# Performance work log

Hardware: AMD Instinct MI355X
Metric: run time of the kernel (lower is better)

## Reference

```python
import jax, jax.numpy as jnp
import numpy as np

# Module config (mirrors PlateYoloBlock __init__)
IMAGE_W, IMAGE_H = 2048, 2048
GRID_SIZE = 8
GRID_W = IMAGE_W // GRID_SIZE  # 256
GRID_H = IMAGE_H // GRID_SIZE  # 256
BBOX_ATTRS = 13


def _xy_offset():
    # np.meshgrid(arange(grid_w), arange(grid_h)) stacked on axis=2 -> (grid_h, grid_w, 2)
    # [..., 0] = x (column) index, [..., 1] = y (row) index
    gx = jnp.arange(GRID_W, dtype=jnp.float32)
    gy = jnp.arange(GRID_H, dtype=jnp.float32)
    xx, yy = jnp.meshgrid(gx, gy)  # each (grid_h, grid_w)
    return jnp.stack([xx, yy], axis=-1)  # (grid_h, grid_w, 2)


def setup_inputs() -> dict:
    key = jax.random.key(0)
    coordinates = jax.random.normal(key, (32, BBOX_ATTRS, GRID_H, GRID_W), dtype=jnp.float32)
    return {"coordinates": coordinates}


def reference(coordinates) -> jnp.ndarray:
    # Inference path of PlateYoloBlock.forward (target=None):
    #   permute (B,13,H,W) -> (B,H,W,13)
    #   xy   = sigmoid(raw[..., :2]) + grid offset
    #   wh   = exp(raw[..., 2:4])
    #   conf = sigmoid(raw[..., -1])
    #   all-but-conf scaled by grid_size; reshape to (B, grid_w*grid_h, 13)
    b = coordinates.shape[0]
    c = jnp.transpose(coordinates, (0, 2, 3, 1))  # (B, grid_h, grid_w, 13)
    xy = jax.nn.sigmoid(c[..., :2]) + _xy_offset()[None]  # (B,H,W,2)
    wh = jnp.exp(c[..., 2:4])
    corners = c[..., 4:12]  # raw 4-corner coords, untouched by activations
    conf = jax.nn.sigmoid(c[..., 12:13])
    boxes = jnp.concatenate([xy, wh, corners], axis=-1) * jnp.float32(GRID_SIZE)
    out = jnp.concatenate([boxes, conf], axis=-1)  # (B,H,W,13)
    return out.reshape(b, GRID_W * GRID_H, BBOX_ATTRS)
```

## Files before the change

kernel.cpp:

```cpp
#include <hip/hip_runtime.h>


#define NB      32
#define NC      13
#define HW      65536
#define WIDTH   256
#define TILE    512
#define THREADS 256

__device__ __forceinline__ float sigmoidf_(float x) {
    return 1.0f / (1.0f + __expf(-x));
}

__global__ __launch_bounds__(THREADS) void plate_yolo_kernel(
        const float* __restrict__ in, float* __restrict__ out) {
    __shared__ float lds[TILE * NC];

    const int tid = threadIdx.x;
    const long long s0 = (long long)blockIdx.x * TILE;
    const int b = (int)(s0 >> 16);
    const int posBase = (int)(s0 & (HW - 1));
    const float* __restrict__ inB = in + (long long)b * NC * HW + posBase;

    #pragma unroll
    for (int k = 0; k < TILE / THREADS; ++k) {
        const int p = tid + k * THREADS;
        const int pos = posBase + p;
        const float fx = (float)(pos & (WIDTH - 1));
        const float fy = (float)(pos >> 8);
        #pragma unroll
        for (int c = 0; c < NC; ++c) {
            float v = inB[c * HW + p];
            float r;
            if (c == 0)                 r = (sigmoidf_(v) + fx) * 8.0f;
            else if (c == 1)            r = (sigmoidf_(v) + fy) * 8.0f;
            else if (c == 2 || c == 3)  r = __expf(v) * 8.0f;
            else if (c == 12)           r = sigmoidf_(v);
            else                        r = v * 8.0f;
            lds[p * NC + c] = r;
        }
    }
    __syncthreads();

    const float4* __restrict__ src = (const float4*)lds;
    float4* __restrict__ dst = (float4*)(out + s0 * NC);
    const int n4 = TILE * NC / 4;
    #pragma unroll
    for (int j = tid; j < n4; j += THREADS) {
        dst[j] = src[j];
    }
}

extern "C" void kernel_launch(void* const* d_in, const int* in_sizes, int n_in,
                              void* d_out, int out_size, void* d_ws, size_t ws_size,
                              hipStream_t stream) {
    const float* in = (const float*)d_in[0];
    float* out = (float*)d_out;
    const int blocks = (NB * HW) / TILE;
    plate_yolo_kernel<<<blocks, THREADS, 0, stream>>>(in, out);
}
```

Baseline: 191.8 us.

## Vectorize loads with float4 per thread and write LDS tile as float4

Each thread now handles four consecutive positions, loading each channel as a float4 so 13 independent wide loads are in flight per thread. Results are packed into registers and stored to LDS as 13 contiguous float4 writes instead of scattered scalar stores. The tile doubles to 1024 positions, which halves the grid and doubles LDS per block (53 KB), possibly reducing occupancy. Per-thread LDS writes at a 52-float stride may cause bank conflicts.

```diff
diff --git a/kernel.cpp b/kernel.cpp
--- a/kernel.cpp
+++ b/kernel.cpp
@@ -5,8 +5,9 @@
 #define NC      13
 #define HW      65536
 #define WIDTH   256
-#define TILE    512
+#define TILE    1024
 #define THREADS 256
+#define PPT     4
 
 __device__ __forceinline__ float sigmoidf_(float x) {
     return 1.0f / (1.0f + __expf(-x));
@@ -22,32 +23,47 @@
     const int posBase = (int)(s0 & (HW - 1));
     const float* __restrict__ inB = in + (long long)b * NC * HW + posBase;
 
+    const int p0   = tid * PPT;
+    const int pos0 = posBase + p0;
+    const float fx0 = (float)(pos0 & (WIDTH - 1));
+    const float fy  = (float)(pos0 >> 8);
+
+    float4 v[NC];
     #pragma unroll
-    for (int k = 0; k < TILE / THREADS; ++k) {
-        const int p = tid + k * THREADS;
-        const int pos = posBase + p;
-        const float fx = (float)(pos & (WIDTH - 1));
-        const float fy = (float)(pos >> 8);
+    for (int c = 0; c < NC; ++c) {
+        v[c] = *(const float4*)(inB + c * HW + p0);
+    }
+
+    float res[PPT * NC];
+    #pragma unroll
+    for (int c = 0; c < NC; ++c) {
+        const float xs[4] = { v[c].x, v[c].y, v[c].z, v[c].w };
         #pragma unroll
-        for (int c = 0; c < NC; ++c) {
-            float v = inB[c * HW + p];
+        for (int q = 0; q < PPT; ++q) {
+            const float x = xs[q];
             float r;
-            if (c == 0)                 r = (sigmoidf_(v) + fx) * 8.0f;
-            else if (c == 1)            r = (sigmoidf_(v) + fy) * 8.0f;
-            else if (c == 2 || c == 3)  r = __expf(v) * 8.0f;
-            else if (c == 12)           r = sigmoidf_(v);
-            else                        r = v * 8.0f;
-            lds[p * NC + c] = r;
+            if (c == 0)                 r = (sigmoidf_(x) + (fx0 + (float)q)) * 8.0f;
+            else if (c == 1)            r = (sigmoidf_(x) + fy) * 8.0f;
+            else if (c == 2 || c == 3)  r = __expf(x) * 8.0f;
+            else if (c == 12)           r = sigmoidf_(x);
+            else                        r = x * 8.0f;
+            res[q * NC + c] = r;
         }
+    }
+
+    float4* __restrict__ ldsT = (float4*)(lds + p0 * NC);
+    #pragma unroll
+    for (int j = 0; j < NC; ++j) {
+        ldsT[j] = make_float4(res[4*j + 0], res[4*j + 1],
+                              res[4*j + 2], res[4*j + 3]);
     }
     __syncthreads();
 
     const float4* __restrict__ src = (const float4*)lds;
     float4* __restrict__ dst = (float4*)(out + s0 * NC);
-    const int n4 = TILE * NC / 4;
     #pragma unroll
-    for (int j = tid; j < n4; j += THREADS) {
-        dst[j] = src[j];
+    for (int j = 0; j < NC; ++j) {
+        dst[tid + j * THREADS] = src[tid + j * THREADS];
     }
 }
 
```

Result: no change. 190.0 us (-0.9%).
